# Kernel tuning notes

Measured on AMD Instinct MI355X. Metric: run time of the kernel, lower is better.

Reference implementation:

```python
import jax, jax.numpy as jnp
import numpy as np

P_SIZES = (1, 2, 4)
O_SIZE = 32
EPS = 1e-5


def bilin_matrix(S, O):
    """Interpolation matrix (O, S) for torch UpsamplingBilinear2d (align_corners=True)."""
    if S == 1:
        return jnp.ones((O, 1), dtype=jnp.float32)
    pos = jnp.arange(O, dtype=jnp.float32) * ((S - 1) / (O - 1))
    lo = jnp.clip(jnp.floor(pos).astype(jnp.int32), 0, S - 2)
    frac = pos - lo.astype(jnp.float32)
    rows = jnp.arange(O)
    M = jnp.zeros((O, S), dtype=jnp.float32)
    M = M.at[rows, lo].add(1.0 - frac).at[rows, lo + 1].add(frac)
    return M


def setup_inputs() -> dict:
    key = jax.random.key(0)
    ks = jax.random.split(key, 12)
    n, C, H = 16, 512, 32
    c4 = C // 4      # 128, value/pyramid channels
    qk = c4 // 8     # 16, query/key channels inside SAE
    s = 0.05
    return {
        "x": jax.random.normal(ks[0], (n, C, H, H), jnp.float32),
        "rce_w": jax.random.normal(ks[1], (3, c4, C), jnp.float32) * s,   # 1x1 conv per pyramid scale
        "rce_b": jax.random.normal(ks[2], (3, c4), jnp.float32) * s,
        "q_w": jax.random.normal(ks[3], (qk, c4), jnp.float32) * s,       # SAE query 1x1 conv
        "q_b": jax.random.normal(ks[4], (qk,), jnp.float32) * s,
        "k_w": jax.random.normal(ks[5], (qk, c4), jnp.float32) * s,       # SAE key 1x1 conv
        "k_b": jax.random.normal(ks[6], (qk,), jnp.float32) * s,
        "value_w": jax.random.normal(ks[7], (c4, C), jnp.float32) * s,    # value 1x1 conv
        "value_b": jax.random.normal(ks[8], (c4,), jnp.float32) * s,
        "fusion_w": jax.random.normal(ks[9], (C, 3 * c4, 3, 3), jnp.float32) * s,  # 3x3 conv, no bias
        "bn_scale": 1.0 + jax.random.normal(ks[10], (C,), jnp.float32) * s,
        "bn_bias": jax.random.normal(ks[11], (C,), jnp.float32) * s,
        "gamma": jnp.asarray(0.5, jnp.float32),
    }


def reference(x, rce_w, rce_b, q_w, q_b, k_w, k_b, value_w, value_b,
              fusion_w, bn_scale, bn_bias, gamma):
    n, C, H, W = x.shape
    c4 = C // 4
    L = H * W

    # value projection: 1x1 conv then flatten -> (n, c4, L)
    proj_value = (jnp.einsum('oc,nchw->nohw', value_w, x)
                  + value_b[None, :, None, None]).reshape(n, c4, L)

    outs = []
    for i, sz in enumerate(P_SIZES):
        # AdaptiveAvgPool2d((sz, sz)) with divisible input -> exact uniform pooling
        pooled = x.reshape(n, C, sz, H // sz, sz, W // sz).mean(axis=(3, 5))
        # 1x1 conv C -> c4
        feat = jnp.einsum('oc,ncij->noij', rce_w[i], pooled) + rce_b[i][None, :, None, None]
        # bilinear upsample (align_corners=True) to (O_SIZE, O_SIZE)
        M = bilin_matrix(sz, O_SIZE)
        up = jnp.einsum('oi,pj,ncij->ncop', M, M, feat)  # (n, c4, H, W)
        # SAE: query/key 1x1 convs, flatten, bmm + softmax
        q = (jnp.einsum('oc,nchw->nohw', q_w, up) + q_b[None, :, None, None]).reshape(n, -1, L)
        k = (jnp.einsum('oc,nchw->nohw', k_w, up) + k_b[None, :, None, None]).reshape(n, -1, L)
        energy = jnp.einsum('ncl,ncm->nlm', q, k)        # (n, L, L)
        attn = jax.nn.softmax(energy, axis=-1)
        # temp = bmm(value, attn^T): temp[c,m] = sum_l value[c,l] * attn[m,l]
        outs.append(jnp.einsum('ncl,nml->ncm', proj_value, attn).reshape(n, c4, H, W))

    cat = jnp.concatenate(outs, axis=1)                  # (n, 3*c4, H, W)
    y = jax.lax.conv_general_dilated(
        cat, fusion_w, window_strides=(1, 1), padding=((1, 1), (1, 1)),
        dimension_numbers=('NCHW', 'OIHW', 'NCHW'))
    # BatchNorm2d in training mode (default): batch statistics over (N, H, W)
    mean = y.mean(axis=(0, 2, 3))
    var = y.var(axis=(0, 2, 3))
    y = (y - mean[None, :, None, None]) * (bn_scale / jnp.sqrt(var + EPS))[None, :, None, None] \
        + bn_bias[None, :, None, None]
    y = jax.nn.relu(y)
    return gamma * y + x
```

## Files before the change

### kernel.cpp

```cpp
#include <hip/hip_runtime.h>
#include <hip/hip_fp16.h>
#include <math.h>

#define OFF_COR   0u
#define OFF_PVH   2097152u
#define OFF_Y     3145728u
#define OFF_CATP  11534336u
#define OFF_QH    15085568u
#define OFF_KH    15347712u
#define OFF_POOL  16134144u
#define OFF_FEAT  16297984u
#define OFF_AW    16338944u
#define OFF_MEANS 17223680u
#define OFF_STAT  17225728u
#define OFF_VWH   17226752u

typedef __bf16 bf16x8 __attribute__((ext_vector_type(8)));
typedef _Float16 f16x8 __attribute__((ext_vector_type(8)));
typedef _Float16 f16x4 __attribute__((ext_vector_type(4)));
typedef float f32x4 __attribute__((ext_vector_type(4)));

__device__ __forceinline__ unsigned short f2bf(float f) {
  unsigned int u = __float_as_uint(f);
  unsigned int r = u + 0x7fff + ((u >> 16) & 1);
  return (unsigned short)(r >> 16);
}

__device__ __forceinline__ unsigned short f2h(float f) {
  union { _Float16 h; unsigned short u; } cv;
  cv.h = (_Float16)f;
  return cv.u;
}

__device__ __forceinline__ void gload_lds16(const void* g, void* l) {
  __builtin_amdgcn_global_load_lds(
      (const __attribute__((address_space(1))) unsigned int*)g,
      (__attribute__((address_space(3))) unsigned int*)l, 16, 0, 0);
}

__global__ __launch_bounds__(256) void pool_kernel(const float* __restrict__ x,
                                                   float* __restrict__ pool) {
  int b = blockIdx.x;
  int t = threadIdx.x;
  const float4* xp = (const float4*)(x + (size_t)b * 1024);
  float4 v = xp[t];
  float s4 = v.x + v.y + v.z + v.w;
  __shared__ float sm[256];
  __shared__ float p4s[16];
  sm[t] = s4;
  __syncthreads();
  if (t < 16) {
    int br = t >> 2, bc = t & 3;
    float s = 0.f;
#pragma unroll
    for (int rr = 0; rr < 8; ++rr) {
      int base = br * 64 + rr * 8 + bc * 2;
      s += sm[base] + sm[base + 1];
    }
    s *= (1.f / 64.f);
    p4s[t] = s;
    pool[(size_t)b * 20 + t] = s;
  }
  __syncthreads();
  if (t < 4) {
    int i2 = t >> 1, j2 = t & 1;
    float s = (p4s[(2*i2)*4 + 2*j2]     + p4s[(2*i2)*4 + 2*j2 + 1] +
               p4s[(2*i2+1)*4 + 2*j2]   + p4s[(2*i2+1)*4 + 2*j2 + 1]) * 0.25f;
    pool[(size_t)b * 20 + 16 + t] = s;
  }
}

__global__ __launch_bounds__(64) void feat_kernel(const float* __restrict__ pool,
                                                  const float* __restrict__ rce_w,
                                                  const float* __restrict__ rce_b,
                                                  float* __restrict__ feat) {
  int o = blockIdx.x, n = blockIdx.y, t = threadIdx.x;
  float part[20];
#pragma unroll
  for (int j = 0; j < 20; ++j) part[j] = 0.f;
  for (int c = t; c < 512; c += 64) {
    const float* pl = pool + ((size_t)n * 512 + c) * 20;
    float w2 = rce_w[(size_t)(128 + o) * 512 + c];
    float w4 = rce_w[(size_t)(256 + o) * 512 + c];
#pragma unroll
    for (int j = 0; j < 4; ++j)  part[j]     += w2 * pl[16 + j];
#pragma unroll
    for (int j = 0; j < 16; ++j) part[4 + j] += w4 * pl[j];
  }
  __shared__ float red[64][20];
#pragma unroll
  for (int j = 0; j < 20; ++j) red[t][j] = part[j];
  __syncthreads();
  if (t < 20) {
    float s = 0.f;
    for (int i = 0; i < 64; ++i) s += red[i][t];
    s += (t < 4) ? rce_b[128 + o] : rce_b[256 + o];
    feat[((size_t)n * 128 + o) * 20 + t] = s;
  }
}

__global__ __launch_bounds__(256) void qk2_kernel(const float* __restrict__ feat,
                                                  const float* __restrict__ q_w,
                                                  const float* __restrict__ q_b,
                                                  const float* __restrict__ k_w,
                                                  const float* __restrict__ k_b,
                                                  unsigned short* __restrict__ qh,
                                                  unsigned short* __restrict__ kh) {
  int n = blockIdx.x, t = threadIdx.x;
  __shared__ float fL[128 * 20];
  __shared__ float GH[2][16][20];
  for (int idx = t; idx < 2560; idx += 256) fL[idx] = feat[(size_t)n * 2560 + idx];
  __syncthreads();
  for (int idx = t; idx < 640; idx += 256) {
    int which = idx / 320, rem = idx % 320, qc = rem / 20, j = rem % 20;
    const float* w = which ? k_w : q_w;
    float s = which ? k_b[qc] : q_b[qc];
    for (int c = 0; c < 128; ++c) s += w[qc * 128 + c] * fL[c * 20 + j];
    GH[which][qc][j] = s;
  }
  __syncthreads();
  for (int it = 0; it < 16; ++it) {
    int row = t + 256 * it;
    int l = row & 1023, which = (row >> 10) & 1, s = row >> 11;
    int ry = l >> 5, cx = l & 31;
    int t0, t1, t2, t3;
    float w0, w1, w2, w3;
    if (s == 0) {
      float a = ry * (1.0f / 31.0f), b = cx * (1.0f / 31.0f);
      t0 = 0; t1 = 1; t2 = 2; t3 = 3;
      w0 = (1.f - a) * (1.f - b); w1 = (1.f - a) * b;
      w2 = a * (1.f - b);         w3 = a * b;
    } else {
      float pr = ry * (3.0f / 31.0f);
      int lr = (int)pr; if (lr > 2) lr = 2;
      float fr = pr - (float)lr;
      float pc = cx * (3.0f / 31.0f);
      int lc = (int)pc; if (lc > 2) lc = 2;
      float fc = pc - (float)lc;
      int base = 4 + lr * 4 + lc;
      t0 = base; t1 = base + 1; t2 = base + 4; t3 = base + 5;
      w0 = (1.f - fr) * (1.f - fc); w1 = (1.f - fr) * fc;
      w2 = fr * (1.f - fc);         w3 = fr * fc;
    }
    float val[16];
#pragma unroll
    for (int qc = 0; qc < 16; ++qc) {
      const float* G = GH[which][qc];
      val[qc] = w0 * G[t0] + w1 * G[t1] + w2 * G[t2] + w3 * G[t3];
    }
    unsigned short* dst = (which ? kh : qh) + (((size_t)(s * 16 + n) * 1024 + l) * 16);
#pragma unroll
    for (int u = 0; u < 4; ++u)
      *(ushort4*)(dst + 4 * u) = make_ushort4(f2h(val[4*u]), f2h(val[4*u+1]),
                                              f2h(val[4*u+2]), f2h(val[4*u+3]));
  }
}

__global__ __launch_bounds__(256) void xcast_kernel(const float* __restrict__ x,
                                                    unsigned short* __restrict__ xT) {
  int lt = blockIdx.x, ct = blockIdx.y, n = blockIdx.z;
  int l0 = lt * 64, c0 = ct * 64, t = threadIdx.x;
  __shared__ float tile[64 * 65];
#pragma unroll
  for (int i = 0; i < 16; ++i) {
    int idx = t + 256 * i;
    int c = idx >> 6, l = idx & 63;
    tile[c * 65 + l] = x[((size_t)n * 512 + c0 + c) * 1024 + l0 + l];
  }
  __syncthreads();
#pragma unroll
  for (int i = 0; i < 16; ++i) {
    int idx = t + 256 * i;
    int l = idx >> 6, c = idx & 63;
    xT[((size_t)n * 1024 + l0 + l) * 512 + c0 + c] = f2h(tile[c * 65 + l]);
  }
}

__global__ __launch_bounds__(256) void vwcast_kernel(const float* __restrict__ vw,
                                                     unsigned short* __restrict__ vwh) {
  int i = blockIdx.x * 256 + threadIdx.x;
  vwh[i] = f2h(vw[i]);
}

__global__ __launch_bounds__(256) void pvmm2_kernel(const unsigned short* __restrict__ vwh,
                                                    const unsigned short* __restrict__ xT,
                                                    const float* __restrict__ vb,
                                                    unsigned short* __restrict__ pvh) {
  int l0 = blockIdx.x * 64;
  int n = blockIdx.y;
  int t = threadIdx.x, lane = t & 63, wv = t >> 6;
  int wm = (wv & 1) * 64, wn = (wv >> 1) * 32;

  __shared__ short Asm[128 * 32];
  __shared__ short Bsm[64 * 32];

  int ar0 = t >> 2,        aq0 = (t & 3) ^ ((ar0 >> 1) & 3);
  int idx1 = t + 256; int ar1 = idx1 >> 2, aq1 = (idx1 & 3) ^ ((ar1 >> 1) & 3);
  int br  = t >> 2,        bq  = (t & 3) ^ ((br >> 1) & 3);
  const unsigned short* Ab0 = vwh + (size_t)ar0 * 512 + aq0 * 8;
  const unsigned short* Ab1 = vwh + (size_t)ar1 * 512 + aq1 * 8;
  const unsigned short* Bb  = xT + ((size_t)n * 1024 + l0 + br) * 512 + bq * 8;
  char* ldsA = (char*)Asm;
  char* ldsB = (char*)Bsm;
  int wvoff = wv * 1024;
  int r15 = lane & 15, kg = lane >> 4;
  int kq = kg ^ ((r15 >> 1) & 3);

  f32x4 acc[4][2];
#pragma unroll
  for (int i = 0; i < 4; ++i)
#pragma unroll
    for (int j = 0; j < 2; ++j) acc[i][j] = (f32x4){0.f, 0.f, 0.f, 0.f};

  for (int k0 = 0; k0 < 512; k0 += 32) {
    __syncthreads();
    gload_lds16(Ab0 + k0, ldsA + wvoff);
    gload_lds16(Ab1 + k0, ldsA + 4096 + wvoff);
    gload_lds16(Bb + k0,  ldsB + wvoff);
    __syncthreads();
    f16x8 af[4], bfr[2];
#pragma unroll
    for (int mt2 = 0; mt2 < 4; ++mt2)
      af[mt2] = *(const f16x8*)&Asm[(wm + mt2 * 16 + r15) * 32 + kq * 8];
#pragma unroll
    for (int nt2 = 0; nt2 < 2; ++nt2)
      bfr[nt2] = *(const f16x8*)&Bsm[(wn + nt2 * 16 + r15) * 32 + kq * 8];
#pragma unroll
    for (int mt2 = 0; mt2 < 4; ++mt2)
#pragma unroll
      for (int nt2 = 0; nt2 < 2; ++nt2)
        acc[mt2][nt2] = __builtin_amdgcn_mfma_f32_16x16x32_f16(af[mt2], bfr[nt2], acc[mt2][nt2], 0, 0, 0);
  }

  int c_lo = wm + (lane >> 4) * 4;
  int l_lo = wn + (lane & 15);
#pragma unroll
  for (int mt2 = 0; mt2 < 4; ++mt2)
#pragma unroll
    for (int nt2 = 0; nt2 < 2; ++nt2) {
      int l = l0 + l_lo + nt2 * 16;
#pragma unroll
      for (int r = 0; r < 4; ++r) {
        int c = c_lo + mt2 * 16 + r;
        pvh[((size_t)n * 128 + c) * 1024 + l] = f2h(acc[mt2][nt2][r] + vb[c]);
      }
    }
}

__global__ __launch_bounds__(256) void mean_kernel(const unsigned short* __restrict__ pvh,
                                                   float* __restrict__ means) {
  int c = blockIdx.x, n = blockIdx.y, t = threadIdx.x;
  f16x4 v = ((const f16x4*)(pvh + ((size_t)n * 128 + c) * 1024))[t];
  float s = (float)v[0] + (float)v[1] + (float)v[2] + (float)v[3];
  for (int o = 32; o > 0; o >>= 1) s += __shfl_down(s, o);
  __shared__ float wsum[4];
  if ((t & 63) == 0) wsum[t >> 6] = s;
  __syncthreads();
  if (t == 0) means[n * 128 + c] = (wsum[0] + wsum[1] + wsum[2] + wsum[3]) * (1.f / 1024.f);
}

__global__ __launch_bounds__(64) void basecor_kernel(const float* __restrict__ means,
                                                     const float* __restrict__ fw,
                                                     float* __restrict__ cor) {
  int oc = blockIdx.x, n = blockIdx.y, t = threadIdx.x;
  float S[9];
#pragma unroll
  for (int j = 0; j < 9; ++j) S[j] = 0.f;
  for (int c = t; c < 128; c += 64) {
    float m = means[n * 128 + c];
    const float* wp = fw + (size_t)oc * 3456 + c * 9;
#pragma unroll
    for (int j = 0; j < 9; ++j) S[j] += m * wp[j];
  }
  __shared__ float red[64][9];
  __shared__ float Sf[9];
#pragma unroll
  for (int j = 0; j < 9; ++j) red[t][j] = S[j];
  __syncthreads();
  if (t < 9) {
    float s = 0.f;
    for (int i = 0; i < 64; ++i) s += red[i][t];
    Sf[t] = s;
  }
  __syncthreads();
  if (t < 9) {
    int a = t / 3, b = t % 3;
    float s = 0.f;
#pragma unroll
    for (int ky = 0; ky < 3; ++ky) {
      if ((a == 0 && ky == 0) || (a == 2 && ky == 2)) continue;
#pragma unroll
      for (int kx = 0; kx < 3; ++kx) {
        if ((b == 0 && kx == 0) || (b == 2 && kx == 2)) continue;
        s += Sf[ky * 3 + kx];
      }
    }
    cor[((size_t)n * 512 + oc) * 9 + t] = s;
  }
}

__global__ __launch_bounds__(128) void fillcat_kernel(unsigned short* __restrict__ catp) {
  int b = blockIdx.x;
  int n = b / 132, e = b % 132;
  int py, px;
  if (e < 34)       { py = 0;          px = e; }
  else if (e < 68)  { py = 33;         px = e - 34; }
  else if (e < 100) { py = e - 68 + 1; px = 0; }
  else              { py = e - 100 + 1; px = 33; }
  unsigned int* row = (unsigned int*)(catp + ((size_t)n * 1156 + py * 34 + px) * 256);
  row[threadIdx.x] = 0u;
}

__global__ __launch_bounds__(256) void wcast_kernel(const float* __restrict__ fw,
                                                    unsigned short* __restrict__ Aw) {
  int oc = blockIdx.x, t = threadIdx.x;
  for (int j = t; j < 2304; j += 256) {
    int seg = j >> 8, ic2 = j & 255;
    Aw[(size_t)oc * 2304 + j] = f2bf(fw[(size_t)oc * 3456 + (128 + ic2) * 9 + seg]);
  }
}

__global__ __launch_bounds__(256) void fattn_kernel(const unsigned short* __restrict__ qh,
                                                    const unsigned short* __restrict__ kh,
                                                    const unsigned short* __restrict__ pvh,
                                                    unsigned short* __restrict__ catp) {
  int m0 = blockIdx.x * 64;
  int n = blockIdx.y, sc = blockIdx.z;
  int t = threadIdx.x, lane = t & 63, wv = t >> 6;
  int wc = (wv >> 1) * 64;
  int wm2 = (wv & 1) * 32;
  int r15 = lane & 15, kg = lane >> 4;
  int kq = kg ^ ((r15 >> 1) & 3);

  const unsigned short* qb  = qh + ((size_t)(sc * 16 + n) * 1024 + m0 + wv * 16) * 16;
  const unsigned short* kb  = kh + ((size_t)(sc * 16 + n) * 1024) * 16;
  const unsigned short* pvb = pvh + (size_t)n * 128 * 1024;

  __shared__ short PVs[2 * 128 * 32];
  __shared__ _Float16 Us[64 * 72];
  __shared__ float rsum[64];

  f16x8 zf = {0, 0, 0, 0, 0, 0, 0, 0};
  f16x8 qa = (kg < 2) ? *(const f16x8*)(qb + r15 * 16 + kg * 8) : zf;

  int prow = t >> 2;
  int aq = (t & 3) ^ ((prow >> 1) & 3);
  const unsigned short* Pb0 = pvb + (size_t)prow * 1024 + aq * 8;
  const unsigned short* Pb1 = pvb + (size_t)(prow + 64) * 1024 + aq * 8;
  char* ldsPV = (char*)PVs;
  int wvoff = wv * 1024;

  f32x4 acc[4][2];
#pragma unroll
  for (int i = 0; i < 4; ++i)
#pragma unroll
    for (int j = 0; j < 2; ++j) acc[i][j] = (f32x4){0.f, 0.f, 0.f, 0.f};
  float rs[4] = {0.f, 0.f, 0.f, 0.f};

  for (int it = 0; it < 16; ++it) {
    int l0 = it * 64;
    __syncthreads();
    gload_lds16(Pb0 + l0,      ldsPV + wvoff);
    gload_lds16(Pb1 + l0,      ldsPV + 4096 + wvoff);
    gload_lds16(Pb0 + l0 + 32, ldsPV + 8192 + wvoff);
    gload_lds16(Pb1 + l0 + 32, ldsPV + 12288 + wvoff);

    f32x4 sacc[4];
#pragma unroll
    for (int lt = 0; lt < 4; ++lt) {
      f16x8 kbf = (kg < 2)
        ? *(const f16x8*)(kb + (size_t)(l0 + lt * 16 + r15) * 16 + kg * 8) : zf;
      sacc[lt] = __builtin_amdgcn_mfma_f32_16x16x32_f16(qa, kbf, (f32x4){0.f,0.f,0.f,0.f}, 0, 0, 0);
    }
#pragma unroll
    for (int lt = 0; lt < 4; ++lt)
#pragma unroll
      for (int r = 0; r < 4; ++r) {
        float e = __expf(sacc[lt][r]);
        Us[(wv * 16 + kg * 4 + r) * 72 + lt * 16 + r15] = (_Float16)e;
        rs[r] += e;
      }
    __syncthreads();

#pragma unroll
    for (int ks = 0; ks < 2; ++ks) {
      f16x8 bfr[2];
#pragma unroll
      for (int nt = 0; nt < 2; ++nt)
        bfr[nt] = *(const f16x8*)&Us[(wm2 + nt * 16 + r15) * 72 + ks * 32 + kg * 8];
#pragma unroll
      for (int ct = 0; ct < 4; ++ct) {
        f16x8 af = *(const f16x8*)&PVs[ks * 4096 + (wc + ct * 16 + r15) * 32 + kq * 8];
#pragma unroll
        for (int nt = 0; nt < 2; ++nt)
          acc[ct][nt] = __builtin_amdgcn_mfma_f32_16x16x32_f16(af, bfr[nt], acc[ct][nt], 0, 0, 0);
      }
    }
  }

#pragma unroll
  for (int r = 0; r < 4; ++r) {
    rs[r] += __shfl_xor(rs[r], 1);
    rs[r] += __shfl_xor(rs[r], 2);
    rs[r] += __shfl_xor(rs[r], 4);
    rs[r] += __shfl_xor(rs[r], 8);
  }
  if (r15 == 0) {
#pragma unroll
    for (int r = 0; r < 4; ++r) rsum[wv * 16 + kg * 4 + r] = rs[r];
  }
  __syncthreads();

#pragma unroll
  for (int nt = 0; nt < 2; ++nt) {
    float inv = 1.f / rsum[wm2 + nt * 16 + r15];
    int pix = m0 + wm2 + nt * 16 + r15;
    unsigned short* ob = catp + ((size_t)n * 1156 + ((pix >> 5) + 1) * 34 + (pix & 31) + 1) * 256
                       + sc * 128 + wc + kg * 4;
#pragma unroll
    for (int ct = 0; ct < 4; ++ct) {
      ushort4 o = make_ushort4(f2bf(acc[ct][nt][0] * inv), f2bf(acc[ct][nt][1] * inv),
                               f2bf(acc[ct][nt][2] * inv), f2bf(acc[ct][nt][3] * inv));
      *(ushort4*)(ob + ct * 16) = o;
    }
  }
}

__global__ __launch_bounds__(256) void convmm_kernel(const unsigned short* __restrict__ Aw,
                                                     const unsigned short* __restrict__ catp,
                                                     const float* __restrict__ cor,
                                                     float* __restrict__ y) {
  int ntile = blockIdx.x;
  int n = ntile >> 3, y0 = (ntile & 7) * 4;
  int m0 = blockIdx.y * 128;
  int t = threadIdx.x;
  int lane = t & 63, wv = t >> 6;
  int wm = (wv & 1) * 64, wn = (wv >> 1) * 64;

  __shared__ short Asm[128 * 32];
  __shared__ short Bsm[128 * 32];

  int idx0 = t, idx1 = t + 256;
  int ar0 = idx0 >> 2, aq0 = (idx0 & 3) ^ ((ar0 >> 1) & 3);
  int ar1 = idx1 >> 2, aq1 = (idx1 & 3) ^ ((ar1 >> 1) & 3);
  size_t abase0 = (size_t)(m0 + ar0) * 2304 + aq0 * 8;
  size_t abase1 = (size_t)(m0 + ar1) * 2304 + aq1 * 8;
  size_t bbase0 = ((size_t)n * 1156 + (size_t)(y0 + (ar0 >> 5)) * 34 + (ar0 & 31)) * 256 + aq0 * 8;
  size_t bbase1 = ((size_t)n * 1156 + (size_t)(y0 + (ar1 >> 5)) * 34 + (ar1 & 31)) * 256 + aq1 * 8;
  char* ldsA = (char*)Asm;
  char* ldsB = (char*)Bsm;
  int wvoff = wv * 1024;

  int r15 = lane & 15, kg = lane >> 4;
  int kq = kg ^ ((r15 >> 1) & 3);

  f32x4 acc[4][4];
#pragma unroll
  for (int i = 0; i < 4; ++i)
#pragma unroll
    for (int j = 0; j < 4; ++j) acc[i][j] = (f32x4){0.f, 0.f, 0.f, 0.f};

  for (int seg = 0; seg < 9; ++seg) {
    size_t boffseg = (size_t)((seg / 3) * 34 + (seg % 3)) * 256;
    size_t akkseg = (size_t)seg * 256;
    for (int icc = 0; icc < 8; ++icc) {
      size_t akk = akkseg + icc * 32;
      size_t boff = boffseg + icc * 32;
      __syncthreads();
      gload_lds16(Aw + abase0 + akk,   ldsA + wvoff);
      gload_lds16(Aw + abase1 + akk,   ldsA + 4096 + wvoff);
      gload_lds16(catp + bbase0 + boff, ldsB + wvoff);
      gload_lds16(catp + bbase1 + boff, ldsB + 4096 + wvoff);
      __syncthreads();
      bf16x8 af[4], bf[4];
#pragma unroll
      for (int mt = 0; mt < 4; ++mt)
        af[mt] = *(const bf16x8*)&Asm[(wm + mt * 16 + r15) * 32 + kq * 8];
#pragma unroll
      for (int nt = 0; nt < 4; ++nt)
        bf[nt] = *(const bf16x8*)&Bsm[(wn + nt * 16 + r15) * 32 + kq * 8];
#pragma unroll
      for (int mt = 0; mt < 4; ++mt)
#pragma unroll
        for (int nt = 0; nt < 4; ++nt)
          acc[mt][nt] = __builtin_amdgcn_mfma_f32_16x16x32_bf16(af[mt], bf[nt], acc[mt][nt], 0, 0, 0);
    }
  }

  int pixbase = (ntile & 7) * 128 + wn + (lane & 15);
  int ocbase = m0 + wm + (lane >> 4) * 4;
#pragma unroll
  for (int mt = 0; mt < 4; ++mt)
#pragma unroll
    for (int nt = 0; nt < 4; ++nt) {
      int oc = ocbase + mt * 16;
      int pix = pixbase + nt * 16;
      int py = pix >> 5, px = pix & 31;
      int yc = (py == 0) ? 0 : ((py == 31) ? 2 : 1);
      int xc = (px == 0) ? 0 : ((px == 31) ? 2 : 1);
      const float* cp = cor + ((size_t)n * 512 + oc) * 9 + yc * 3 + xc;
      float* yp = y + ((size_t)n * 512 + oc) * 1024 + pix;
#pragma unroll
      for (int r = 0; r < 4; ++r) yp[(size_t)r * 1024] = acc[mt][nt][r] + cp[(size_t)r * 9];
    }
}

__global__ __launch_bounds__(256) void bnstat_kernel(const float* __restrict__ y,
                                                     const float* __restrict__ bn_scale,
                                                     const float* __restrict__ bn_bias,
                                                     float* __restrict__ stats) {
  int oc = blockIdx.x, t = threadIdx.x;
  float s = 0.f, ss = 0.f;
  for (int n = 0; n < 16; ++n) {
    float4 v = ((const float4*)(y + ((size_t)n * 512 + oc) * 1024))[t];
    s  += v.x + v.y + v.z + v.w;
    ss += v.x * v.x + v.y * v.y + v.z * v.z + v.w * v.w;
  }
  for (int o = 32; o > 0; o >>= 1) {
    s  += __shfl_down(s, o);
    ss += __shfl_down(ss, o);
  }
  __shared__ float rs[4], rss[4];
  if ((t & 63) == 0) { rs[t >> 6] = s; rss[t >> 6] = ss; }
  __syncthreads();
  if (t == 0) {
    float S = rs[0] + rs[1] + rs[2] + rs[3];
    float SS = rss[0] + rss[1] + rss[2] + rss[3];
    float mean = S * (1.f / 16384.f);
    float var = SS * (1.f / 16384.f) - mean * mean;
    float se = bn_scale[oc] / sqrtf(var + 1e-5f);
    stats[oc * 2] = se;
    stats[oc * 2 + 1] = bn_bias[oc] - mean * se;
  }
}

__global__ __launch_bounds__(256) void final_kernel(const float* __restrict__ y,
                                                    const float* __restrict__ x,
                                                    const float* __restrict__ stats,
                                                    const float* __restrict__ gamma,
                                                    float* __restrict__ outp) {
  int b = blockIdx.x;
  int c = b & 511;
  int t = threadIdx.x;
  float se = stats[c * 2], sh = stats[c * 2 + 1], g = gamma[0];
  float4 yv = ((const float4*)(y + (size_t)b * 1024))[t];
  float4 xv = ((const float4*)(x + (size_t)b * 1024))[t];
  float4 o;
  o.x = g * fmaxf(yv.x * se + sh, 0.f) + xv.x;
  o.y = g * fmaxf(yv.y * se + sh, 0.f) + xv.y;
  o.z = g * fmaxf(yv.z * se + sh, 0.f) + xv.z;
  o.w = g * fmaxf(yv.w * se + sh, 0.f) + xv.w;
  ((float4*)(outp + (size_t)b * 1024))[t] = o;
}

extern "C" void kernel_launch(void* const* d_in, const int* in_sizes, int n_in,
                              void* d_out, int out_size, void* d_ws, size_t ws_size,
                              hipStream_t stream) {
  const float* x        = (const float*)d_in[0];
  const float* rce_w    = (const float*)d_in[1];
  const float* rce_b    = (const float*)d_in[2];
  const float* q_w      = (const float*)d_in[3];
  const float* q_b      = (const float*)d_in[4];
  const float* k_w      = (const float*)d_in[5];
  const float* k_b      = (const float*)d_in[6];
  const float* value_w  = (const float*)d_in[7];
  const float* value_b  = (const float*)d_in[8];
  const float* fw       = (const float*)d_in[9];
  const float* bn_scale = (const float*)d_in[10];
  const float* bn_bias  = (const float*)d_in[11];
  const float* gamma    = (const float*)d_in[12];

  float* ws    = (float*)d_ws;
  float* cor   = ws + OFF_COR;
  unsigned short* pvh = (unsigned short*)(ws + OFF_PVH);
  float* ybuf  = ws + OFF_Y;
  unsigned short* xTbuf = (unsigned short*)(ws + OFF_Y);
  unsigned short* catp = (unsigned short*)(ws + OFF_CATP);
  unsigned short* qh   = (unsigned short*)(ws + OFF_QH);
  unsigned short* kh   = (unsigned short*)(ws + OFF_KH);
  float* pool  = ws + OFF_POOL;
  float* feat  = ws + OFF_FEAT;
  unsigned short* Aw = (unsigned short*)(ws + OFF_AW);
  float* means = ws + OFF_MEANS;
  float* stats = ws + OFF_STAT;
  unsigned short* vwh = (unsigned short*)(ws + OFF_VWH);
  float* outp  = (float*)d_out;

  hipLaunchKernelGGL(pool_kernel,    dim3(8192),       dim3(256), 0, stream, x, pool);
  hipLaunchKernelGGL(feat_kernel,    dim3(128, 16),    dim3(64),  0, stream, pool, rce_w, rce_b, feat);
  hipLaunchKernelGGL(qk2_kernel,     dim3(16),         dim3(256), 0, stream, feat, q_w, q_b, k_w, k_b, qh, kh);
  hipLaunchKernelGGL(xcast_kernel,   dim3(16, 8, 16),  dim3(256), 0, stream, x, xTbuf);
  hipLaunchKernelGGL(vwcast_kernel,  dim3(256),        dim3(256), 0, stream, value_w, vwh);
  hipLaunchKernelGGL(pvmm2_kernel,   dim3(16, 16),     dim3(256), 0, stream, vwh, xTbuf, value_b, pvh);
  hipLaunchKernelGGL(mean_kernel,    dim3(128, 16),    dim3(256), 0, stream, pvh, means);
  hipLaunchKernelGGL(basecor_kernel, dim3(512, 16),    dim3(64),  0, stream, means, fw, cor);
  hipLaunchKernelGGL(fillcat_kernel, dim3(2112),       dim3(128), 0, stream, catp);
  hipLaunchKernelGGL(wcast_kernel,   dim3(512),        dim3(256), 0, stream, fw, Aw);
  hipLaunchKernelGGL(fattn_kernel,   dim3(16, 16, 2),  dim3(256), 0, stream, qh, kh, pvh, catp);
  hipLaunchKernelGGL(convmm_kernel,  dim3(128, 4),     dim3(256), 0, stream, Aw, catp, cor, ybuf);
  hipLaunchKernelGGL(bnstat_kernel,  dim3(512),        dim3(256), 0, stream, ybuf, bn_scale, bn_bias, stats);
  hipLaunchKernelGGL(final_kernel,   dim3(8192),       dim3(256), 0, stream, ybuf, x, stats, gamma, outp);
}
```

Baseline: 264.9 us.

## Double-buffer conv GEMM LDS tiles and double K-step per barrier

The 3x3 conv implicit GEMM now uses two LDS buffers. Each stage loads 64 K-elements (two 32-wide subtiles) for both operands. The global-to-LDS loads for the next stage are issued before computing on the current one, so there is one barrier per stage instead of two barriers per 32-K step. This aims to hide global load latency and cut synchronisation overhead, at the cost of four times the LDS per block, which may reduce occupancy.

```diff
diff --git a/kernel.cpp b/kernel.cpp
--- a/kernel.cpp
+++ b/kernel.cpp
@@ -426,6 +426,41 @@
   }
 }
 
+__device__ __forceinline__ void conv_stage(const unsigned short* __restrict__ Aw,
+                                           const unsigned short* __restrict__ catp,
+                                           size_t abase0, size_t abase1,
+                                           size_t bbase0, size_t bbase1,
+                                           int s, char* la, char* lb, int wvoff) {
+  int seg = s >> 2;
+  size_t akk  = (size_t)s * 64;
+  size_t boff = (size_t)((seg / 3) * 34 + (seg % 3)) * 256 + (size_t)(s & 3) * 64;
+  gload_lds16(Aw + abase0 + akk,          la + wvoff);
+  gload_lds16(Aw + abase1 + akk,          la + 4096 + wvoff);
+  gload_lds16(Aw + abase0 + akk + 32,     la + 8192 + wvoff);
+  gload_lds16(Aw + abase1 + akk + 32,     la + 12288 + wvoff);
+  gload_lds16(catp + bbase0 + boff,       lb + wvoff);
+  gload_lds16(catp + bbase1 + boff,       lb + 4096 + wvoff);
+  gload_lds16(catp + bbase0 + boff + 32,  lb + 8192 + wvoff);
+  gload_lds16(catp + bbase1 + boff + 32,  lb + 12288 + wvoff);
+}
+
+__device__ __forceinline__ void conv_comp(const short* As_, const short* Bs_,
+                                          int wm, int wn, int r15, int kq,
+                                          f32x4 acc[4][4]) {
+  bf16x8 af[4], bf[4];
+#pragma unroll
+  for (int mt = 0; mt < 4; ++mt)
+    af[mt] = *(const bf16x8*)&As_[(wm + mt * 16 + r15) * 32 + kq * 8];
+#pragma unroll
+  for (int nt = 0; nt < 4; ++nt)
+    bf[nt] = *(const bf16x8*)&Bs_[(wn + nt * 16 + r15) * 32 + kq * 8];
+#pragma unroll
+  for (int mt = 0; mt < 4; ++mt)
+#pragma unroll
+    for (int nt = 0; nt < 4; ++nt)
+      acc[mt][nt] = __builtin_amdgcn_mfma_f32_16x16x32_bf16(af[mt], bf[nt], acc[mt][nt], 0, 0, 0);
+}
+
 __global__ __launch_bounds__(256) void convmm_kernel(const unsigned short* __restrict__ Aw,
                                                      const unsigned short* __restrict__ catp,
                                                      const float* __restrict__ cor,
@@ -437,8 +472,8 @@
   int lane = t & 63, wv = t >> 6;
   int wm = (wv & 1) * 64, wn = (wv >> 1) * 64;
 
-  __shared__ short Asm[128 * 32];
-  __shared__ short Bsm[128 * 32];
+  __shared__ short Asm[2 * 2 * 128 * 32];
+  __shared__ short Bsm[2 * 2 * 128 * 32];
 
   int idx0 = t, idx1 = t + 256;
   int ar0 = idx0 >> 2, aq0 = (idx0 & 3) ^ ((ar0 >> 1) & 3);
@@ -460,31 +495,19 @@
 #pragma unroll
     for (int j = 0; j < 4; ++j) acc[i][j] = (f32x4){0.f, 0.f, 0.f, 0.f};
 
-  for (int seg = 0; seg < 9; ++seg) {
-    size_t boffseg = (size_t)((seg / 3) * 34 + (seg % 3)) * 256;
-    size_t akkseg = (size_t)seg * 256;
-    for (int icc = 0; icc < 8; ++icc) {
-      size_t akk = akkseg + icc * 32;
-      size_t boff = boffseg + icc * 32;
-      __syncthreads();
-      gload_lds16(Aw + abase0 + akk,   ldsA + wvoff);
-      gload_lds16(Aw + abase1 + akk,   ldsA + 4096 + wvoff);
-      gload_lds16(catp + bbase0 + boff, ldsB + wvoff);
-      gload_lds16(catp + bbase1 + boff, ldsB + 4096 + wvoff);
-      __syncthreads();
-      bf16x8 af[4], bf[4];
-#pragma unroll
-      for (int mt = 0; mt < 4; ++mt)
-        af[mt] = *(const bf16x8*)&Asm[(wm + mt * 16 + r15) * 32 + kq * 8];
-#pragma unroll
-      for (int nt = 0; nt < 4; ++nt)
-        bf[nt] = *(const bf16x8*)&Bsm[(wn + nt * 16 + r15) * 32 + kq * 8];
-#pragma unroll
-      for (int mt = 0; mt < 4; ++mt)
-#pragma unroll
-        for (int nt = 0; nt < 4; ++nt)
-          acc[mt][nt] = __builtin_amdgcn_mfma_f32_16x16x32_bf16(af[mt], bf[nt], acc[mt][nt], 0, 0, 0);
-    }
+  conv_stage(Aw, catp, abase0, abase1, bbase0, bbase1, 0, ldsA, ldsB, wvoff);
+  __syncthreads();
+
+#pragma unroll 2
+  for (int s = 0; s < 36; ++s) {
+    char* la = ldsA + (s & 1) * 16384;
+    char* lb = ldsB + (s & 1) * 16384;
+    if (s < 35)
+      conv_stage(Aw, catp, abase0, abase1, bbase0, bbase1, s + 1,
+                 ldsA + ((s + 1) & 1) * 16384, ldsB + ((s + 1) & 1) * 16384, wvoff);
+    conv_comp((const short*)la,          (const short*)lb,          wm, wn, r15, kq, acc);
+    conv_comp((const short*)(la + 8192), (const short*)(lb + 8192), wm, wn, r15, kq, acc);
+    __syncthreads();
   }
 
   int pixbase = (ntile & 7) * 128 + wn + (lane & 15);
```

Result: faster. 259.7 us (-2.0%).

## Stage padded image tile in LDS and reuse it across all nine conv taps

Applied to the files above, without the earlier changes.

The implicit-GEMM 3x3 conv kernel now loads a 6x34-pixel by 64-channel slab of the padded input into LDS once per channel group and reads all nine shifted taps from it, instead of reloading B from global memory for every tap. The weight matrix is reordered to a group-tap-channel layout, and A tiles are double-buffered with a prefetch of the next tap's K=64 slice. This removes redundant global loads of the input and halves the number of barriers per K step. The cost is a larger LDS footprint, which may lower occupancy, plus a stall when the image slab is reloaded at each group boundary.

```diff
diff --git a/kernel.cpp b/kernel.cpp
--- a/kernel.cpp
+++ b/kernel.cpp
@@ -315,8 +315,10 @@
                                                     unsigned short* __restrict__ Aw) {
   int oc = blockIdx.x, t = threadIdx.x;
   for (int j = t; j < 2304; j += 256) {
-    int seg = j >> 8, ic2 = j & 255;
-    Aw[(size_t)oc * 2304 + j] = f2bf(fw[(size_t)oc * 3456 + (128 + ic2) * 9 + seg]);
+    int g = j / 576, r = j % 576;
+    int tap = r >> 6, i = r & 63;
+    Aw[(size_t)oc * 2304 + j] =
+        f2bf(fw[(size_t)oc * 3456 + (size_t)(128 + g * 64 + i) * 9 + tap]);
   }
 }
 
@@ -437,53 +439,88 @@
   int lane = t & 63, wv = t >> 6;
   int wm = (wv & 1) * 64, wn = (wv >> 1) * 64;
 
-  __shared__ short Asm[128 * 32];
-  __shared__ short Bsm[128 * 32];
+  __shared__ short Asm[2 * 2 * 128 * 32];
+  __shared__ short Bimg[208 * 64];
 
   int idx0 = t, idx1 = t + 256;
   int ar0 = idx0 >> 2, aq0 = (idx0 & 3) ^ ((ar0 >> 1) & 3);
   int ar1 = idx1 >> 2, aq1 = (idx1 & 3) ^ ((ar1 >> 1) & 3);
   size_t abase0 = (size_t)(m0 + ar0) * 2304 + aq0 * 8;
   size_t abase1 = (size_t)(m0 + ar1) * 2304 + aq1 * 8;
-  size_t bbase0 = ((size_t)n * 1156 + (size_t)(y0 + (ar0 >> 5)) * 34 + (ar0 & 31)) * 256 + aq0 * 8;
-  size_t bbase1 = ((size_t)n * 1156 + (size_t)(y0 + (ar1 >> 5)) * 34 + (ar1 & 31)) * 256 + aq1 * 8;
   char* ldsA = (char*)Asm;
-  char* ldsB = (char*)Bsm;
+  char* ldsB = (char*)Bimg;
   int wvoff = wv * 1024;
+
+  const unsigned short* cb = catp + ((size_t)n * 1156 + (size_t)y0 * 34) * 256;
+  int bpx = lane >> 3;
+  int bch = (lane & 7) ^ (bpx & 7);
 
   int r15 = lane & 15, kg = lane >> 4;
   int kq = kg ^ ((r15 >> 1) & 3);
 
+  int pxl[4];
+#pragma unroll
+  for (int nt = 0; nt < 4; ++nt) {
+    int pn = wn + nt * 16 + r15;
+    pxl[nt] = (pn >> 5) * 34 + (pn & 31);
+  }
+
   f32x4 acc[4][4];
 #pragma unroll
   for (int i = 0; i < 4; ++i)
 #pragma unroll
     for (int j = 0; j < 4; ++j) acc[i][j] = (f32x4){0.f, 0.f, 0.f, 0.f};
 
-  for (int seg = 0; seg < 9; ++seg) {
-    size_t boffseg = (size_t)((seg / 3) * 34 + (seg % 3)) * 256;
-    size_t akkseg = (size_t)seg * 256;
-    for (int icc = 0; icc < 8; ++icc) {
-      size_t akk = akkseg + icc * 32;
-      size_t boff = boffseg + icc * 32;
+  for (int j = wv; j < 26; j += 4)
+    gload_lds16(cb + (size_t)(j * 8 + bpx) * 256 + bch * 8, ldsB + j * 1024);
+  gload_lds16(Aw + abase0,      ldsA + wvoff);
+  gload_lds16(Aw + abase1,      ldsA + 4096 + wvoff);
+  gload_lds16(Aw + abase0 + 32, ldsA + 8192 + wvoff);
+  gload_lds16(Aw + abase1 + 32, ldsA + 12288 + wvoff);
+  __syncthreads();
+
+  int q = 0;
+  for (int g = 0; g < 4; ++g) {
+    for (int tap = 0; tap < 9; ++tap, ++q) {
+      char* la = ldsA + (q & 1) * 16384;
+      if (q < 35) {
+        int tapn = tap + 1, gn = g;
+        if (tapn == 9) { tapn = 0; gn = g + 1; }
+        size_t akk = (size_t)(gn * 576 + tapn * 64);
+        char* ln = ldsA + ((q + 1) & 1) * 16384;
+        gload_lds16(Aw + abase0 + akk,      ln + wvoff);
+        gload_lds16(Aw + abase1 + akk,      ln + 4096 + wvoff);
+        gload_lds16(Aw + abase0 + akk + 32, ln + 8192 + wvoff);
+        gload_lds16(Aw + abase1 + akk + 32, ln + 12288 + wvoff);
+      }
+      int sy = tap / 3;
+      int toff = sy * 34 + (tap - sy * 3);
+#pragma unroll
+      for (int c = 0; c < 2; ++c) {
+        const short* As_ = (const short*)(la + c * 8192);
+        bf16x8 af[4], bfv[4];
+#pragma unroll
+        for (int mt = 0; mt < 4; ++mt)
+          af[mt] = *(const bf16x8*)&As_[(wm + mt * 16 + r15) * 32 + kq * 8];
+#pragma unroll
+        for (int nt = 0; nt < 4; ++nt) {
+          int px = pxl[nt] + toff;
+          int lch = (c * 4 + kg) ^ (px & 7);
+          bfv[nt] = *(const bf16x8*)&Bimg[px * 64 + lch * 8];
+        }
+#pragma unroll
+        for (int mt = 0; mt < 4; ++mt)
+#pragma unroll
+          for (int nt = 0; nt < 4; ++nt)
+            acc[mt][nt] = __builtin_amdgcn_mfma_f32_16x16x32_bf16(af[mt], bfv[nt], acc[mt][nt], 0, 0, 0);
+      }
       __syncthreads();
-      gload_lds16(Aw + abase0 + akk,   ldsA + wvoff);
-      gload_lds16(Aw + abase1 + akk,   ldsA + 4096 + wvoff);
-      gload_lds16(catp + bbase0 + boff, ldsB + wvoff);
-      gload_lds16(catp + bbase1 + boff, ldsB + 4096 + wvoff);
-      __syncthreads();
-      bf16x8 af[4], bf[4];
-#pragma unroll
-      for (int mt = 0; mt < 4; ++mt)
-        af[mt] = *(const bf16x8*)&Asm[(wm + mt * 16 + r15) * 32 + kq * 8];
-#pragma unroll
-      for (int nt = 0; nt < 4; ++nt)
-        bf[nt] = *(const bf16x8*)&Bsm[(wn + nt * 16 + r15) * 32 + kq * 8];
-#pragma unroll
-      for (int mt = 0; mt < 4; ++mt)
-#pragma unroll
-        for (int nt = 0; nt < 4; ++nt)
-          acc[mt][nt] = __builtin_amdgcn_mfma_f32_16x16x32_bf16(af[mt], bf[nt], acc[mt][nt], 0, 0, 0);
+      if (tap == 8 && g < 3) {
+        for (int j = wv; j < 26; j += 4)
+          gload_lds16(cb + (size_t)(j * 8 + bpx) * 256 + (g + 1) * 64 + bch * 8,
+                      ldsB + j * 1024);
+        __syncthreads();
+      }
     }
   }
 
```

New measurement: 259.3 us. 2.1% less time.
